# Performance work log

Hardware: AMD Instinct MI355X
Metric: run time of the kernel (lower is better)

## Reference

```python
import jax, jax.numpy as jnp
import numpy as np

B, T, F, V, NTXT = 32, 1, 1, 729, 64
DIM, DIM_LLM = 1152, 4096
HEADS, DIM_HEAD, DEPTH, NUM_LATENTS, FF_MULT = 16, 96, 6, 64, 4
INNER = HEADS * DIM_HEAD
FF_INNER = DIM * FF_MULT
SCALE = DIM_HEAD ** -0.5


def _ln(x, w, b, eps=1e-5):
    mu = x.mean(-1, keepdims=True)
    var = ((x - mu) ** 2).mean(-1, keepdims=True)
    return (x - mu) * jax.lax.rsqrt(var + eps) * w + b


def setup_inputs() -> dict:
    key = jax.random.key(0)
    ks = jax.random.split(key, 12)
    w = lambda k, shape: jax.random.normal(k, shape, dtype=jnp.float32) * 0.02
    return {
        "x": jax.random.normal(ks[0], (B, T, F, V, DIM), dtype=jnp.float32),
        "text_embeds": jax.random.normal(ks[1], (B, NTXT, DIM_LLM), dtype=jnp.float32),
        "latents": jax.random.normal(ks[2], (NUM_LATENTS, DIM), dtype=jnp.float32),
        "txt_w1": w(ks[3], (DIM_LLM, DIM)),
        "txt_b1": jnp.zeros((DIM,), jnp.float32),
        "txt_w2": w(ks[4], (DIM, DIM)),
        "txt_b2": jnp.zeros((DIM,), jnp.float32),
        "nm_w": jnp.ones((DEPTH, DIM), jnp.float32),
        "nm_b": jnp.zeros((DEPTH, DIM), jnp.float32),
        "nl_w": jnp.ones((DEPTH, DIM), jnp.float32),
        "nl_b": jnp.zeros((DEPTH, DIM), jnp.float32),
        "Wq": w(ks[5], (DEPTH, DIM, INNER)),
        "Wkv": w(ks[6], (DEPTH, DIM, 2 * INNER)),
        "Wo": w(ks[7], (DEPTH, INNER, DIM)),
        "ffln_w": jnp.ones((DEPTH, DIM), jnp.float32),
        "ffln_b": jnp.zeros((DEPTH, DIM), jnp.float32),
        "ff_w1": w(ks[8], (DEPTH, DIM, FF_INNER)),
        "ff_w2": w(ks[9], (DEPTH, FF_INNER, DIM)),
        "out_ln_w": jnp.ones((DIM,), jnp.float32),
        "out_ln_b": jnp.zeros((DIM,), jnp.float32),
    }


def reference(x, text_embeds, latents, txt_w1, txt_b1, txt_w2, txt_b2,
              nm_w, nm_b, nl_w, nl_b, Wq, Wkv, Wo,
              ffln_w, ffln_b, ff_w1, ff_w2, out_ln_w, out_ln_b):
    b, t, f, v, d = x.shape
    xf = x.reshape(b, t, f * v, d)  # (b, T, F*v, D)
    # text_projection: Linear -> GELU -> Linear
    txt = jax.nn.gelu(text_embeds @ txt_w1 + txt_b1, approximate=False) @ txt_w2 + txt_b2
    lat = jnp.broadcast_to(latents, (b, t, NUM_LATENTS, d))
    lat = jnp.concatenate(
        [lat, jnp.broadcast_to(txt[:, None], (b, t, txt.shape[1], d))], axis=2)
    n2 = lat.shape[2]
    for i in range(DEPTH):
        # PerceiverAttention
        xm = _ln(xf, nm_w[i], nm_b[i])
        lm = _ln(lat, nl_w[i], nl_b[i])
        q = (lm @ Wq[i]).reshape(b, t, n2, HEADS, DIM_HEAD)
        kv = jnp.concatenate([xm, lm], axis=2) @ Wkv[i]
        k, v_ = jnp.split(kv, 2, axis=-1)
        nk = k.shape[2]
        k = k.reshape(b, t, nk, HEADS, DIM_HEAD)
        v_ = v_.reshape(b, t, nk, HEADS, DIM_HEAD)
        sim = jnp.einsum('btihd,btjhd->bthij', q * SCALE, k)
        attn = jax.nn.softmax(sim, axis=-1)  # stable softmax == amax subtract + softmax
        out = jnp.einsum('bthij,btjhd->btihd', attn, v_).reshape(b, t, n2, INNER) @ Wo[i]
        lat = out + lat
        # FeedForward: LN -> Linear -> GELU -> Linear, residual
        lat = jax.nn.gelu(_ln(lat, ffln_w[i], ffln_b[i]) @ ff_w1[i],
                          approximate=False) @ ff_w2[i] + lat
    lat = lat[:, :, :NUM_LATENTS, :]
    return _ln(lat, out_ln_w, out_ln_b)
```

## Files before the change

### kernel.cpp

```cpp
#include <hip/hip_runtime.h>
#include <hip/hip_bf16.h>
#include <math.h>


typedef __attribute__((ext_vector_type(4))) float f32x4;
typedef __attribute__((ext_vector_type(8))) short bf16x8;
typedef unsigned int u32;

#define DEV __device__ __forceinline__

DEV float bf2f(short s){ union{u32 u; float f;} v; v.u = ((u32)(unsigned short)s) << 16; return v.f; }
DEV short f2bf(float f){
  union{float f; u32 u;} v; v.f = f;
  u32 r = (v.u + 0x7FFFu + ((v.u >> 16) & 1u)) >> 16;
  return (short)r;
}

DEV u32 lds_off(const short* p){
  return (u32)(uintptr_t)(__attribute__((address_space(3))) const short*)p;
}
template<int OFF>
DEV bf16x8 dsro(u32 addr){
  bf16x8 r;
  asm volatile("ds_read_b128 %0, %1 offset:%2" : "=v"(r) : "v"(addr), "i"(OFF));
  return r;
}

template<int GELU, int BIAS, int OUTF32, int CMAP, int KSPLIT>
__global__ __launch_bounds__(512, 4)
void gemm_v2(const short* __restrict__ A, const short* __restrict__ Bm,
             void* __restrict__ Cv, short* __restrict__ C2,
             const float* __restrict__ bias,
             int K, int lda, int ldb, int ldc,
             int Mvalid, int NBmax, int Nwrite)
{
  __shared__ __align__(16) short LDS[36864];

  int Mb = gridDim.x;
  int nwg = gridDim.x * gridDim.y;
  int bid = blockIdx.y * gridDim.x + blockIdx.x;
  int m0, n0;
  if ((Mb & 7) == 0){
    int mslab = Mb >> 3;
    int c = bid & 7, s = bid >> 3;
    int ml = s % mslab, nl = s / mslab;
    m0 = (c*mslab + ml) * 128;
    n0 = nl * 256;
  } else if ((nwg & 7) == 0){
    int chunk = nwg >> 3;
    int b2 = (bid & 7)*chunk + (bid >> 3);
    int by = b2 / Mb;
    m0 = (b2 - by*Mb) * 128;
    n0 = by * 256;
  } else {
    m0 = blockIdx.x * 128;
    n0 = blockIdx.y * 256;
  }
  int kzoff = KSPLIT ? (int)blockIdx.z * K : 0;

  int tid = threadIdx.x, lane = tid & 63, w = tid >> 6;
  int wr = w >> 2, wc = w & 3;
  int rsel = lane & 15, g4 = lane >> 4;

  int sl = lane >> 3;
  int l  = (lane & 7) ^ sl;
  int lc = (l & 3) * 8;
  int lh = l >> 2;
  const short* gA;
  { int r = m0 + w*8 + sl + lh*64; if (r > Mvalid-1) r = Mvalid-1;
    gA = A + (long)r*lda + lc + kzoff; }
  const short* gB0;
  { int r = n0 + w*8 + sl + lh*128; if (r > NBmax-1) r = NBmax-1;
    gB0 = Bm + (long)r*ldb + lc + kzoff; }
  const short* gB1;
  { int r = n0 + 64 + w*8 + sl + lh*128; if (r > NBmax-1) r = NBmax-1;
    gB1 = Bm + (long)r*ldb + lc + kzoff; }
  char* dA  = (char*)LDS + w*1024;
  char* dB0 = (char*)LDS + 8192  + w*1024;
  char* dB1 = (char*)LDS + 16384 + w*1024;

#define GLDS(src, dst) __builtin_amdgcn_global_load_lds( \
      (const __attribute__((address_space(1))) u32*)(src), \
      (__attribute__((address_space(3))) u32*)(dst), 16, 0, 0)
#define STAGE(bo, tau) do { \
    int kb = (tau)*32; \
    GLDS(gA  + kb, dA  + (bo)); \
    GLDS(gB0 + kb, dB0 + (bo)); \
    GLDS(gB1 + kb, dB1 + (bo)); \
  } while(0)

  u32 base = lds_off(LDS);
  u32 aAddr = base + (u32)(rsel*128 + (((wr*4 + g4) ^ (rsel & 7))*16));
  u32 bAddr = base + 8192u
            + (u32)(((wc & 1)*64 + rsel)*128 + ((((wc >> 1)*4 + g4) ^ (rsel & 7))*16));

  int nt = K >> 5;

  f32x4 acc[4][4];
#pragma unroll
  for (int i=0;i<4;i++)
#pragma unroll
    for (int j=0;j<4;j++) acc[i][j] = (f32x4){0.f,0.f,0.f,0.f};

  STAGE(0u, 0);
  if (nt > 1) STAGE(24576u, 1);

  u32 boCur = 0;
#pragma unroll 1
  for (int t=0; t<nt; ++t){
    if (t == nt-1) { asm volatile("s_waitcnt vmcnt(0)" ::: "memory"); }
    else           { asm volatile("s_waitcnt vmcnt(3)" ::: "memory"); }
    asm volatile("s_barrier" ::: "memory");
    u32 aa = aAddr + boCur, bb = bAddr + boCur;
    bf16x8 af[4], bfr[4];
    af[0]  = dsro<0>(aa);    af[1]  = dsro<2048>(aa);
    af[2]  = dsro<4096>(aa); af[3]  = dsro<6144>(aa);
    bfr[0] = dsro<0>(bb);    bfr[1] = dsro<2048>(bb);
    bfr[2] = dsro<4096>(bb); bfr[3] = dsro<6144>(bb);
    if (t+2 < nt){
      u32 boN2 = boCur + 49152u; if (boN2 >= 73728u) boN2 -= 73728u;
      STAGE(boN2, t+2);
    }
    asm volatile("s_waitcnt lgkmcnt(0)" ::: "memory");
    __builtin_amdgcn_sched_barrier(0);
    __builtin_amdgcn_s_setprio(1);
#pragma unroll
    for (int mi=0; mi<4; mi++)
#pragma unroll
      for (int nn=0; nn<4; nn++)
        acc[mi][nn] = __builtin_amdgcn_mfma_f32_16x16x32_bf16(af[mi], bfr[nn], acc[mi][nn], 0, 0, 0);
    __builtin_amdgcn_s_setprio(0);
    boCur += 24576u; if (boCur == 73728u) boCur = 0;
  }
#undef STAGE
#undef GLDS

  int cq = g4 * 4;
  int csel = rsel;
#pragma unroll
  for (int mi=0; mi<4; mi++){
#pragma unroll
    for (int nn=0; nn<4; nn++){
#pragma unroll
      for (int j=0; j<4; j++){
        int gm = m0 + wr*64 + mi*16 + cq + j;
        int gn = n0 + wc*64 + nn*16 + csel;
        if (gm < Mvalid && gn < Nwrite){
          float v = acc[mi][nn][j];
          if (BIAS) v += bias[gn];
          if (GELU) v = 0.5f*v*(1.0f + erff(v*0.70710678118654752f));
          if (CMAP == 0){
            long off = (long)gm*ldc + gn;
            if (KSPLIT) off += (long)blockIdx.z * ((long)Mvalid * ldc);
            if (OUTF32) ((float*)Cv)[off] = v;
            else        ((short*)Cv)[off] = f2bf(v);
          } else if (CMAP == 1){
            int bb2 = gm / 729;
            int jj = gm - bb2*729;
            ((short*)Cv)[((long)bb2*857 + jj)*3072 + gn] = f2bf(v);
          } else {
            if (gn < 1536){
              ((short*)Cv)[(long)gm*1536 + gn] = f2bf(v * 0.1020620726159657f);
            } else {
              int bb2 = gm >> 7, jj = gm & 127;
              C2[((long)bb2*857 + 729 + jj)*3072 + (gn - 1536)] = f2bf(v);
            }
          }
        }
      }
    }
  }
}

__global__ __launch_bounds__(256)
void red2_ln(float* __restrict__ lat, const float* __restrict__ p, long n,
             short* __restrict__ lm, const float* __restrict__ w,
             const float* __restrict__ b)
{
  const int D = 1152;
  int r = blockIdx.x;
  long rb = (long)r*D;
  int tid = threadIdx.x;
  float s1=0.f, s2=0.f;
  float xv[5];
#pragma unroll
  for (int t=0;t<5;t++){
    int i = tid + t*256;
    float v = 0.f;
    if (i < D){
      v = lat[rb+i] + p[rb+i] + p[n+rb+i];
      lat[rb+i] = v;
    }
    xv[t] = v; s1 += v; s2 += v*v;
  }
  if (!w) return;
#pragma unroll
  for (int o=32;o;o>>=1){ s1 += __shfl_xor(s1,o); s2 += __shfl_xor(s2,o); }
  __shared__ float red[8];
  int wid = tid>>6, lane = tid&63;
  if (lane==0){ red[wid]=s1; red[4+wid]=s2; }
  __syncthreads();
  s1 = red[0]+red[1]+red[2]+red[3];
  s2 = red[4]+red[5]+red[6]+red[7];
  float mu = s1 / D;
  float var = s2 / D - mu*mu;
  float rs = rsqrtf(var + 1e-5f);
#pragma unroll
  for (int t=0;t<5;t++){
    int i = tid + t*256;
    if (i >= D) break;
    lm[rb+i] = f2bf((xv[t]-mu)*rs*w[i] + b[i]);
  }
}

__global__ __launch_bounds__(256)
void flash_attn(const short* __restrict__ qb, const short* __restrict__ kv,
                short* __restrict__ attn)
{
  __shared__ short Kt[96][104];
  __shared__ short Vs[96][104];
  __shared__ short Pb[4][32][104];
  __shared__ float FAC[128];

  int z = blockIdx.x;
  int b = z >> 4, h = z & 15;
  int tid = threadIdx.x;
  int lane = tid & 63;
  int w = tid >> 6;
  int l15 = lane & 15, g4 = lane >> 4;

  bf16x8 qf[2][3];
#pragma unroll
  for (int n=0;n<2;n++)
#pragma unroll
    for (int kf=0;kf<3;kf++)
      qf[n][kf] = *(const bf16x8*)&qb[((long)(b*128 + w*32 + n*16 + l15))*1536
                                     + h*96 + kf*32 + g4*8];

  f32x4 acc[2][6];
#pragma unroll
  for (int i=0;i<2;i++)
#pragma unroll
    for (int j=0;j<6;j++) acc[i][j] = (f32x4){0.f,0.f,0.f,0.f};
  float m_run[2] = {-1e30f, -1e30f};
  float l_run[2] = {0.f, 0.f};

  const short* kvb = kv + (long)b*857*3072 + h*96;
  const short* vvb = kvb + 1536;

  for (int t=0; t<9; ++t){
    int k0 = t*96;
    for (int c = tid; c < 1152; c += 256){
      int r = c / 12;
      int c12 = c - r*12;
      int key = k0 + r; if (key > 856) key = 856;
      *(bf16x8*)&Kt[r][c12*8] = *(const bf16x8*)&kvb[(long)key*3072 + c12*8];
      bf16x8 vv = *(const bf16x8*)&vvb[(long)key*3072 + c12*8];
#pragma unroll
      for (int j=0;j<8;j++) Vs[c12*8 + j][r] = ((short*)&vv)[j];
    }
    __syncthreads();

    f32x4 st[6][2];
#pragma unroll
    for (int m=0;m<6;m++){ st[m][0]=(f32x4){0,0,0,0}; st[m][1]=(f32x4){0,0,0,0}; }
#pragma unroll
    for (int kf=0;kf<3;kf++){
      bf16x8 af[6];
#pragma unroll
      for (int m=0;m<6;m++) af[m] = *(const bf16x8*)&Kt[m*16 + l15][kf*32 + g4*8];
#pragma unroll
      for (int m=0;m<6;m++){
        st[m][0] = __builtin_amdgcn_mfma_f32_16x16x32_bf16(af[m], qf[0][kf], st[m][0], 0,0,0);
        st[m][1] = __builtin_amdgcn_mfma_f32_16x16x32_bf16(af[m], qf[1][kf], st[m][1], 0,0,0);
      }
    }

    if (k0 + 96 > 857){
#pragma unroll
      for (int m=0;m<6;m++)
#pragma unroll
        for (int j=0;j<4;j++){
          if (k0 + m*16 + g4*4 + j > 856){ st[m][0][j] = -1e30f; st[m][1][j] = -1e30f; }
        }
    }

#pragma unroll
    for (int n=0;n<2;n++){
      float mx = -1e30f;
#pragma unroll
      for (int m=0;m<6;m++)
#pragma unroll
        for (int j=0;j<4;j++) mx = fmaxf(mx, st[m][n][j]);
      mx = fmaxf(mx, __shfl_xor(mx, 16));
      mx = fmaxf(mx, __shfl_xor(mx, 32));
      float mn = fmaxf(m_run[n], mx);
      float f  = __expf(m_run[n] - mn);
      m_run[n] = mn;
      float s = 0.f;
#pragma unroll
      for (int m=0;m<6;m++)
#pragma unroll
        for (int j=0;j<4;j++){
          float e = __expf(st[m][n][j] - mn);
          st[m][n][j] = e; s += e;
        }
      s += __shfl_xor(s, 16);
      s += __shfl_xor(s, 32);
      l_run[n] = l_run[n]*f + s;
      if (g4 == 0) FAC[w*32 + n*16 + l15] = f;
    }

#pragma unroll
    for (int m=0;m<6;m++)
#pragma unroll
      for (int n=0;n<2;n++){
        short4 pk;
        pk.x = f2bf(st[m][n][0]); pk.y = f2bf(st[m][n][1]);
        pk.z = f2bf(st[m][n][2]); pk.w = f2bf(st[m][n][3]);
        *(short4*)&Pb[w][n*16 + l15][m*16 + g4*4] = pk;
      }

    {
      float4 fj0 = *(const float4*)&FAC[w*32 +  0 + g4*4];
      float4 fj1 = *(const float4*)&FAC[w*32 + 16 + g4*4];
#pragma unroll
      for (int nn=0;nn<6;nn++){
        acc[0][nn][0] *= fj0.x; acc[0][nn][1] *= fj0.y;
        acc[0][nn][2] *= fj0.z; acc[0][nn][3] *= fj0.w;
        acc[1][nn][0] *= fj1.x; acc[1][nn][1] *= fj1.y;
        acc[1][nn][2] *= fj1.z; acc[1][nn][3] *= fj1.w;
      }
    }

#pragma unroll
    for (int kf=0;kf<3;kf++){
      bf16x8 pa0 = *(const bf16x8*)&Pb[w][ 0 + l15][kf*32 + g4*8];
      bf16x8 pa1 = *(const bf16x8*)&Pb[w][16 + l15][kf*32 + g4*8];
#pragma unroll
      for (int nn=0;nn<6;nn++){
        bf16x8 vb = *(const bf16x8*)&Vs[nn*16 + l15][kf*32 + g4*8];
        acc[0][nn] = __builtin_amdgcn_mfma_f32_16x16x32_bf16(pa0, vb, acc[0][nn], 0,0,0);
        acc[1][nn] = __builtin_amdgcn_mfma_f32_16x16x32_bf16(pa1, vb, acc[1][nn], 0,0,0);
      }
    }
    __syncthreads();
  }

  if (g4 == 0){
    FAC[w*32 +  0 + l15] = 1.0f / l_run[0];
    FAC[w*32 + 16 + l15] = 1.0f / l_run[1];
  }
  float4 li0 = *(const float4*)&FAC[w*32 +  0 + g4*4];
  float4 li1 = *(const float4*)&FAC[w*32 + 16 + g4*4];
  float li[2][4] = {{li0.x,li0.y,li0.z,li0.w},{li1.x,li1.y,li1.z,li1.w}};
#pragma unroll
  for (int mo=0;mo<2;mo++)
#pragma unroll
    for (int nn=0;nn<6;nn++)
#pragma unroll
      for (int j=0;j<4;j++){
        int q = w*32 + mo*16 + g4*4 + j;
        int d = nn*16 + l15;
        attn[((long)(b*128+q))*1536 + h*96 + d] = f2bf(acc[mo][nn][j]*li[mo][j]);
      }
}

template<int GELU, int BIAS, int RES, int OUTF32>
__global__ __launch_bounds__(256)
void gemm_t(const short* __restrict__ A, const short* __restrict__ B,
            void* __restrict__ C, const float* __restrict__ bias,
            const float* __restrict__ res,
            int K, int lda, int ldb, int ldc,
            int Mvalid, int NBmax, int Nwrite,
            int zdiv, long sA1, long sA2, long sB1, long sB2, long sC1, long sC2,
            float scale)
{
  __shared__ __align__(16) short As[2][128*32];
  __shared__ __align__(16) short Bs[2][128*32];

  int z = blockIdx.z;
  int zq = z / zdiv, zr = z - zq*zdiv;
  const short* Ab = A + zq*sA1 + zr*sA2;
  const short* Bb = B + zq*sB1 + zr*sB2;
  long cOff = zq*sC1 + zr*sC2;
  int m0 = blockIdx.y * 128;
  int n0 = blockIdx.x * 128;
  int tid = threadIdx.x;
  int lane = tid & 63;
  int w = tid >> 6;
  int wm = (w >> 1) * 64, wn = (w & 1) * 64;

  int sr = lane >> 2;
  int sc = (lane & 3) * 8;
  int ar0 = m0 + w*32 + sr;
  int br0 = n0 + w*32 + sr;

  int raA0 = ar0;      if (raA0 > Mvalid-1) raA0 = Mvalid-1;
  int raA1 = ar0 + 16; if (raA1 > Mvalid-1) raA1 = Mvalid-1;
  int rbB0 = br0;      if (rbB0 > NBmax-1) rbB0 = NBmax-1;
  int rbB1 = br0 + 16; if (rbB1 > NBmax-1) rbB1 = NBmax-1;
  const short* gA0 = Ab + (long)raA0*lda + sc;
  const short* gA1 = Ab + (long)raA1*lda + sc;
  const short* gB0 = Bb + (long)rbB0*ldb + sc;
  const short* gB1 = Bb + (long)rbB1*ldb + sc;
  int ldsRow0 = (w*32)*32;
  int ldsRow1 = (w*32 + 16)*32;

  f32x4 acc[4][4];
#pragma unroll
  for (int i=0;i<4;i++)
#pragma unroll
    for (int j=0;j<4;j++) acc[i][j] = (f32x4){0.f,0.f,0.f,0.f};

  auto stage = [&](int buf, int kb){
    __builtin_amdgcn_global_load_lds(
        (const __attribute__((address_space(1))) u32*)(gA0 + kb),
        (__attribute__((address_space(3))) u32*)(&As[buf][ldsRow0]), 16, 0, 0);
    __builtin_amdgcn_global_load_lds(
        (const __attribute__((address_space(1))) u32*)(gA1 + kb),
        (__attribute__((address_space(3))) u32*)(&As[buf][ldsRow1]), 16, 0, 0);
    __builtin_amdgcn_global_load_lds(
        (const __attribute__((address_space(1))) u32*)(gB0 + kb),
        (__attribute__((address_space(3))) u32*)(&Bs[buf][ldsRow0]), 16, 0, 0);
    __builtin_amdgcn_global_load_lds(
        (const __attribute__((address_space(1))) u32*)(gB1 + kb),
        (__attribute__((address_space(3))) u32*)(&Bs[buf][ldsRow1]), 16, 0, 0);
  };

  int nt = K >> 5;
  stage(0, 0);
  __syncthreads();

  int kq = (lane >> 4) * 8;
  int rsel = lane & 15;
  int cur = 0;
  for (int t = 0; t < nt; ++t){
    if (t + 1 < nt) stage(cur ^ 1, (t+1)*32);

    bf16x8 af[4], bfr[4];
#pragma unroll
    for (int m=0;m<4;m++) af[m]  = *(const bf16x8*)&As[cur][(wm + m*16 + rsel)*32 + kq];
#pragma unroll
    for (int n=0;n<4;n++) bfr[n] = *(const bf16x8*)&Bs[cur][(wn + n*16 + rsel)*32 + kq];
#pragma unroll
    for (int m=0;m<4;m++)
#pragma unroll
      for (int n=0;n<4;n++)
        acc[m][n] = __builtin_amdgcn_mfma_f32_16x16x32_bf16(af[m], bfr[n], acc[m][n], 0, 0, 0);

    __syncthreads();
    cur ^= 1;
  }

  int cq = (lane >> 4) * 4;
  int csel = lane & 15;
#pragma unroll
  for (int m=0;m<4;m++){
#pragma unroll
    for (int n=0;n<4;n++){
#pragma unroll
      for (int j=0;j<4;j++){
        int gm = m0 + wm + m*16 + cq + j;
        int gn = n0 + wn + n*16 + csel;
        if (gm < Mvalid && gn < Nwrite){
          float v = acc[m][n][j] * scale;
          if (BIAS) v += bias[gn];
          if (GELU) v = 0.5f*v*(1.0f + erff(v*0.70710678118654752f));
          long off = cOff + (long)gm*ldc + gn;
          if (OUTF32){
            float rv = RES ? res[off] : 0.0f;
            ((float*)C)[off] = v + rv;
          } else {
            ((short*)C)[off] = f2bf(v);
          }
        }
      }
    }
  }
}

__global__ __launch_bounds__(256)
void convT(const float* __restrict__ in, short* __restrict__ out,
           int K, int N, const float* __restrict__ s)
{
  __shared__ float tile[32][33];
  int kb = blockIdx.y*32, nb = blockIdx.x*32;
  int tx = threadIdx.x & 31, ty = threadIdx.x >> 5;
  for (int i = ty; i < 32; i += 8){
    int k = kb + i, n = nb + tx;
    float v = 0.f;
    if (k < K && n < N){ v = in[(long)k*N + n]; if (s) v *= s[k]; }
    tile[i][tx] = v;
  }
  __syncthreads();
  for (int i = ty; i < 32; i += 8){
    int n = nb + i, k = kb + tx;
    if (n < N && k < K) out[(long)n*K + k] = f2bf(tile[tx][i]);
  }
}

__global__ __launch_bounds__(256)
void convT_qkv(const float* __restrict__ Wq, const float* __restrict__ Wkv,
               const float* __restrict__ s,
               short* __restrict__ outQ, short* __restrict__ outKx,
               short* __restrict__ outK)
{
  __shared__ float tile[32][33];
  __shared__ float sv[32];
  int b = blockIdx.x;
  int tx = threadIdx.x & 31, ty = threadIdx.x >> 5;
  if (b < 1728){
    int bx = b % 48, byy = b / 48;
    int kb = byy*32, nb = bx*32;
    for (int i = ty; i < 32; i += 8)
      tile[i][tx] = Wq[(long)(kb + i)*1536 + nb + tx];
    __syncthreads();
    for (int i = ty; i < 32; i += 8)
      outQ[(long)(nb + i)*1152 + kb + tx] = f2bf(tile[tx][i]);
  } else {
    int b2 = b - 1728;
    int bx = b2 % 96, byy = b2 / 96;
    int kb = byy*32, nb = bx*32;
    if (threadIdx.x < 32) sv[threadIdx.x] = s[kb + threadIdx.x];
    for (int i = ty; i < 32; i += 8)
      tile[i][tx] = Wkv[(long)(kb + i)*3072 + nb + tx];
    __syncthreads();
    for (int i = ty; i < 32; i += 8){
      float v = tile[tx][i];
      long o = (long)(nb + i)*1152 + kb + tx;
      outK[o]  = f2bf(v);
      outKx[o] = f2bf(v * sv[tx]);
    }
  }
}

__global__ __launch_bounds__(256)
void convT_ffo(const float* __restrict__ Wo, const float* __restrict__ fw1,
               const float* __restrict__ fw2,
               short* __restrict__ outWo, short* __restrict__ outF1,
               short* __restrict__ outF2)
{
  __shared__ float tile[32][33];
  int b = blockIdx.x;
  int tx = threadIdx.x & 31, ty = threadIdx.x >> 5;
  const float* in; short* out; int K, N, kb, nb;
  if (b < 1728){
    in = Wo; out = outWo; K = 1536; N = 1152;
    nb = (b % 36)*32; kb = (b / 36)*32;
  } else if (b < 6912){
    int b2 = b - 1728;
    in = fw1; out = outF1; K = 1152; N = 4608;
    nb = (b2 % 144)*32; kb = (b2 / 144)*32;
  } else {
    int b3 = b - 6912;
    in = fw2; out = outF2; K = 4608; N = 1152;
    nb = (b3 % 36)*32; kb = (b3 / 36)*32;
  }
  for (int i = ty; i < 32; i += 8)
    tile[i][tx] = in[(long)(kb + i)*N + nb + tx];
  __syncthreads();
  for (int i = ty; i < 32; i += 8)
    out[(long)(nb + i)*K + kb + tx] = f2bf(tile[tx][i]);
}

__global__ __launch_bounds__(256)
void biasfold6(const float* __restrict__ Wkv, const float* __restrict__ nm_b,
               float* __restrict__ outb)
{
  int L = blockIdx.y;
  int n = blockIdx.x*256 + threadIdx.x;
  const float* W = Wkv + (size_t)L*1152*3072;
  const float* bvec = nm_b + L*1152;
  float s = 0.f;
  for (int k=0;k<1152;k++) s += bvec[k]*W[(long)k*3072 + n];
  outb[L*3072 + n] = s;
}

__global__ __launch_bounds__(256)
void cvt_bf16x4(const float* __restrict__ in, short* __restrict__ o, long n)
{
  long i = ((long)blockIdx.x*256 + threadIdx.x)*4;
  if (i >= n) return;
  float4 v = *(const float4*)(in + i);
  short4 s4;
  s4.x = f2bf(v.x); s4.y = f2bf(v.y); s4.z = f2bf(v.z); s4.w = f2bf(v.w);
  *(short4*)&o[i] = s4;
}

__global__ __launch_bounds__(256)
void latcopy(const float* __restrict__ latents, float* __restrict__ lat)
{
  int idx = blockIdx.x*256 + threadIdx.x;
  int d = idx % 1152; int j = (idx / 1152) % 64; int b = idx / (1152*64);
  lat[((long)b*128 + j)*1152 + d] = latents[j*1152 + d];
}

template<int OUTF32>
__global__ __launch_bounds__(256)
void ln_k(const float* __restrict__ in, void* __restrict__ outp,
          const float* __restrict__ w, const float* __restrict__ b,
          int grpSel, int grpStride)
{
  const int D = 1152;
  int r = blockIdx.x;
  long ir = (long)(r / grpSel)*grpStride + (r % grpSel);
  const float* x = in + ir*D;
  int tid = threadIdx.x;
  float s1=0.f, s2=0.f;
  float xv[5];
#pragma unroll
  for (int t=0;t<5;t++){
    int i = tid + t*256;
    xv[t] = (i < D) ? x[i] : 0.f;
    s1 += xv[t]; s2 += xv[t]*xv[t];
  }
#pragma unroll
  for (int o=32;o;o>>=1){ s1 += __shfl_xor(s1,o); s2 += __shfl_xor(s2,o); }
  __shared__ float red[8];
  int wid = tid>>6, lane = tid&63;
  if (lane==0){ red[wid]=s1; red[4+wid]=s2; }
  __syncthreads();
  s1 = red[0]+red[1]+red[2]+red[3];
  s2 = red[4]+red[5]+red[6]+red[7];
  float mu = s1 / D;
  float var = s2 / D - mu*mu;
  float rs = rsqrtf(var + 1e-5f);
#pragma unroll
  for (int t=0;t<5;t++){
    int i = tid + t*256;
    if (i >= D) break;
    float v = (xv[t]-mu)*rs;
    if (w) v = v*w[i] + b[i];
    if (OUTF32) ((float*)outp)[(long)r*D + i] = v;
    else        ((short*)outp)[(long)r*D + i] = f2bf(v);
  }
}


extern "C" void kernel_launch(void* const* d_in, const int* in_sizes, int n_in,
                              void* d_out, int out_size, void* d_ws, size_t ws_size,
                              hipStream_t stream)
{
  const float* x      = (const float*)d_in[0];
  const float* tein   = (const float*)d_in[1];
  const float* lat0   = (const float*)d_in[2];
  const float* txt_w1 = (const float*)d_in[3];
  const float* txt_b1 = (const float*)d_in[4];
  const float* txt_w2 = (const float*)d_in[5];
  const float* txt_b2 = (const float*)d_in[6];
  const float* nm_w   = (const float*)d_in[7];
  const float* nm_b   = (const float*)d_in[8];
  const float* nl_w   = (const float*)d_in[9];
  const float* nl_b   = (const float*)d_in[10];
  const float* Wq     = (const float*)d_in[11];
  const float* Wkv    = (const float*)d_in[12];
  const float* Wo     = (const float*)d_in[13];
  const float* ffln_w = (const float*)d_in[14];
  const float* ffln_b = (const float*)d_in[15];
  const float* ff_w1  = (const float*)d_in[16];
  const float* ff_w2  = (const float*)d_in[17];
  const float* oln_w  = (const float*)d_in[18];
  const float* oln_b  = (const float*)d_in[19];
  float* out = (float*)d_out;
  (void)in_sizes; (void)n_in; (void)out_size; (void)ws_size;

  char* base = (char*)d_ws;
  size_t off = 0;
  auto alloc = [&](size_t bytes)->char*{
    char* r = base + off;
    off += (bytes + 255) & ~(size_t)255;
    return r;
  };
  short* wT    = (short*)alloc(4608ULL*1152*2);
  short* wTx   = (short*)alloc(3072ULL*1152*2);
  short* wTo   = (short*)alloc(1152ULL*1536*2);
  short* wTf1  = (short*)alloc(4608ULL*1152*2);
  short* wTf2  = (short*)alloc(1152ULL*4608*2);
  float* biasf = (float*)alloc(6*3072*4);
  float* ppart = (float*)alloc(2ULL*4096*1152*4);
  short* xnorm = (short*)alloc(23328ULL*1152*2);
  float* lat   = (float*)alloc(4096ULL*1152*4);
  short* lm    = (short*)alloc(4096ULL*1152*2);
  short* qb    = (short*)alloc(4096ULL*1536*2);
  short* kv    = (short*)alloc(27424ULL*3072*2);
  short* SP    = (short*)alloc(2048ULL*4096*2 + 2048ULL*1152*2);
  short* attn  = (short*)alloc(4096ULL*1536*2);
  short* ffh   = (short*)alloc(4096ULL*4608*2);
  short* txtin = SP;
  short* txth  = SP + 2048ULL*4096;

  cvt_bf16x4<<<8192,256,0,stream>>>(tein, txtin, 2048LL*4096);
  convT<<<dim3(36,128),256,0,stream>>>(txt_w1, wT, 4096, 1152, nullptr);
  gemm_t<1,1,0,0><<<dim3(9,16,1),256,0,stream>>>(txtin, wT, txth, txt_b1, nullptr,
      4096,4096,4096,1152, 2048,1152,1152, 1, 0,0,0,0,0,0, 1.f);
  convT<<<dim3(36,36),256,0,stream>>>(txt_w2, wT, 1152, 1152, nullptr);
  gemm_t<0,1,0,1><<<dim3(9,1,32),256,0,stream>>>(txth, wT, lat + 64*1152, txt_b2, nullptr,
      1152,1152,1152,1152, 64,1152,1152, 1, 64L*1152,0, 0,0, 128L*1152,0, 1.f);
  latcopy<<<9216,256,0,stream>>>(lat0, lat);

  ln_k<0><<<23328,256,0,stream>>>(x, xnorm, nullptr, nullptr, 1<<28, 0);
  ln_k<0><<<4096,256,0,stream>>>(lat, lm, nl_w, nl_b, 1<<28, 0);
  biasfold6<<<dim3(12,6),256,0,stream>>>(Wkv, nm_b, biasf);

  for (int L=0; L<6; L++){
    const float* WqL  = Wq    + (size_t)L*1152*1536;
    const float* WkvL = Wkv   + (size_t)L*1152*3072;
    const float* WoL  = Wo    + (size_t)L*1536*1152;
    const float* fw1  = ff_w1 + (size_t)L*1152*4608;
    const float* fw2  = ff_w2 + (size_t)L*4608*1152;
    int Ln = (L+1 < 6) ? (L+1) : 5;

    convT_qkv<<<5184,256,0,stream>>>(WqL, WkvL, nm_w + L*1152,
        wT, wTx, wT + 1536*1152);

    gemm_v2<0,0,0,2,0><<<dim3(32,18),512,0,stream>>>(lm, wT, qb, kv, nullptr,
        1152,1152,1152,0, 4096, 4608, 4608);

    gemm_v2<0,1,0,1,0><<<dim3(184,12),512,0,stream>>>(xnorm, wTx, kv, nullptr,
        biasf + L*3072, 1152,1152,1152,0, 23328, 3072, 3072);

    flash_attn<<<512,256,0,stream>>>(qb, kv, attn);

    convT_ffo<<<12096,256,0,stream>>>(WoL, fw1, fw2, wTo, wTf1, wTf2);

    gemm_v2<0,0,1,0,1><<<dim3(32,5,2),512,0,stream>>>(attn, wTo, ppart, nullptr, nullptr,
        768,1536,1536,1152, 4096, 1152, 1152);
    red2_ln<<<4096,256,0,stream>>>(lat, ppart, 4096L*1152, lm,
        ffln_w + L*1152, ffln_b + L*1152);

    gemm_v2<1,0,0,0,0><<<dim3(32,18),512,0,stream>>>(lm, wTf1, ffh, nullptr, nullptr,
        1152,1152,1152,4608, 4096, 4608, 4608);
    gemm_v2<0,0,1,0,1><<<dim3(32,5,2),512,0,stream>>>(ffh, wTf2, ppart, nullptr, nullptr,
        2304,4608,4608,1152, 4096, 1152, 1152);
    red2_ln<<<4096,256,0,stream>>>(lat, ppart, 4096L*1152, lm,
        (L+1 < 6) ? (nl_w + Ln*1152) : nullptr, nl_b + Ln*1152);
  }

  ln_k<1><<<2048,256,0,stream>>>(lat, out, oln_w, oln_b, 64, 128);
}
```

Measured before the change: 3.670 ms.

## Merge per-layer weight transposes and fuse Q/KV GEMMs into one launch

Combines the two per-layer weight conversion kernels into a single launch covering Wq, Wkv, Wo and both FF weights. Replaces the two separate GEMM launches, one for the latent Q/KV projection and one for the x KV projection, with a single grouped GEMM kernel. That kernel assigns blocks to either problem by block index, remaps block order into XCD-strided slabs, and uses a triple-buffered global-to-LDS pipeline. The aim is to cut launch overhead and tail underutilisation and to improve L2 locality, at the cost of a more specialised kernel with hard-coded shapes.

```diff
diff --git a/kernel.cpp b/kernel.cpp
--- a/kernel.cpp
+++ b/kernel.cpp
@@ -172,6 +172,143 @@
   }
 }
 
+__global__ __launch_bounds__(512, 4)
+void gemm_qkvx(const short* __restrict__ lm, const short* __restrict__ xnorm,
+               const short* __restrict__ wTq, const short* __restrict__ wTx,
+               short* __restrict__ qb, short* __restrict__ kv,
+               const float* __restrict__ biasL)
+{
+  __shared__ __align__(16) short LDS[36864];
+
+  int bid = blockIdx.x;
+  int which = (bid >= 576);
+  const short* A; const short* Bm;
+  int m0, n0, Mvalid, NBmax;
+  if (!which){
+    int mslab = 4;
+    int c = bid & 7, s = bid >> 3;
+    m0 = (c*mslab + s % mslab) * 128;
+    n0 = (s / mslab) * 256;
+    A = lm; Bm = wTq; Mvalid = 4096; NBmax = 4608;
+  } else {
+    int local = bid - 576;
+    int mslab = 23;
+    int c = local & 7, s = local >> 3;
+    m0 = (c*mslab + s % mslab) * 128;
+    n0 = (s / mslab) * 256;
+    A = xnorm; Bm = wTx; Mvalid = 23328; NBmax = 3072;
+  }
+
+  int tid = threadIdx.x, lane = tid & 63, w = tid >> 6;
+  int wr = w >> 2, wc = w & 3;
+  int rsel = lane & 15, g4 = lane >> 4;
+
+  int sl = lane >> 3;
+  int l  = (lane & 7) ^ sl;
+  int lc = (l & 3) * 8;
+  int lh = l >> 2;
+  const short* gA;
+  { int r = m0 + w*8 + sl + lh*64; if (r > Mvalid-1) r = Mvalid-1;
+    gA = A + (long)r*1152 + lc; }
+  const short* gB0;
+  { int r = n0 + w*8 + sl + lh*128; if (r > NBmax-1) r = NBmax-1;
+    gB0 = Bm + (long)r*1152 + lc; }
+  const short* gB1;
+  { int r = n0 + 64 + w*8 + sl + lh*128; if (r > NBmax-1) r = NBmax-1;
+    gB1 = Bm + (long)r*1152 + lc; }
+  char* dA  = (char*)LDS + w*1024;
+  char* dB0 = (char*)LDS + 8192  + w*1024;
+  char* dB1 = (char*)LDS + 16384 + w*1024;
+
+#define GLDS(src, dst) __builtin_amdgcn_global_load_lds( \
+      (const __attribute__((address_space(1))) u32*)(src), \
+      (__attribute__((address_space(3))) u32*)(dst), 16, 0, 0)
+#define STAGE(bo, tau) do { \
+    int kb = (tau)*32; \
+    GLDS(gA  + kb, dA  + (bo)); \
+    GLDS(gB0 + kb, dB0 + (bo)); \
+    GLDS(gB1 + kb, dB1 + (bo)); \
+  } while(0)
+
+  u32 base = lds_off(LDS);
+  u32 aAddr = base + (u32)(rsel*128 + (((wr*4 + g4) ^ (rsel & 7))*16));
+  u32 bAddr = base + 8192u
+            + (u32)(((wc & 1)*64 + rsel)*128 + ((((wc >> 1)*4 + g4) ^ (rsel & 7))*16));
+
+  const int nt = 36;
+
+  f32x4 acc[4][4];
+#pragma unroll
+  for (int i=0;i<4;i++)
+#pragma unroll
+    for (int j=0;j<4;j++) acc[i][j] = (f32x4){0.f,0.f,0.f,0.f};
+
+  STAGE(0u, 0);
+  STAGE(24576u, 1);
+
+  u32 boCur = 0;
+#pragma unroll 1
+  for (int t=0; t<nt; ++t){
+    if (t == nt-1) { asm volatile("s_waitcnt vmcnt(0)" ::: "memory"); }
+    else           { asm volatile("s_waitcnt vmcnt(3)" ::: "memory"); }
+    asm volatile("s_barrier" ::: "memory");
+    u32 aa = aAddr + boCur, bb = bAddr + boCur;
+    bf16x8 af[4], bfr[4];
+    af[0]  = dsro<0>(aa);    af[1]  = dsro<2048>(aa);
+    af[2]  = dsro<4096>(aa); af[3]  = dsro<6144>(aa);
+    bfr[0] = dsro<0>(bb);    bfr[1] = dsro<2048>(bb);
+    bfr[2] = dsro<4096>(bb); bfr[3] = dsro<6144>(bb);
+    if (t+2 < nt){
+      u32 boN2 = boCur + 49152u; if (boN2 >= 73728u) boN2 -= 73728u;
+      STAGE(boN2, t+2);
+    }
+    asm volatile("s_waitcnt lgkmcnt(0)" ::: "memory");
+    __builtin_amdgcn_sched_barrier(0);
+    __builtin_amdgcn_s_setprio(1);
+#pragma unroll
+    for (int mi=0; mi<4; mi++)
+#pragma unroll
+      for (int nn=0; nn<4; nn++)
+        acc[mi][nn] = __builtin_amdgcn_mfma_f32_16x16x32_bf16(af[mi], bfr[nn], acc[mi][nn], 0, 0, 0);
+    __builtin_amdgcn_s_setprio(0);
+    boCur += 24576u; if (boCur == 73728u) boCur = 0;
+  }
+#undef STAGE
+#undef GLDS
+
+  int cq = g4 * 4;
+  int csel = rsel;
+#pragma unroll
+  for (int mi=0; mi<4; mi++){
+#pragma unroll
+    for (int nn=0; nn<4; nn++){
+#pragma unroll
+      for (int j=0; j<4; j++){
+        int gm = m0 + wr*64 + mi*16 + cq + j;
+        int gn = n0 + wc*64 + nn*16 + csel;
+        if (!which){
+          if (gm < 4096 && gn < 4608){
+            float v = acc[mi][nn][j];
+            if (gn < 1536){
+              qb[(long)gm*1536 + gn] = f2bf(v * 0.1020620726159657f);
+            } else {
+              int bb2 = gm >> 7, jj = gm & 127;
+              kv[((long)bb2*857 + 729 + jj)*3072 + (gn - 1536)] = f2bf(v);
+            }
+          }
+        } else {
+          if (gm < 23328 && gn < 3072){
+            float v = acc[mi][nn][j] + biasL[gn];
+            int bb2 = gm / 729;
+            int jj = gm - bb2*729;
+            kv[((long)bb2*857 + jj)*3072 + gn] = f2bf(v);
+          }
+        }
+      }
+    }
+  }
+}
+
 __global__ __launch_bounds__(256)
 void red2_ln(float* __restrict__ lat, const float* __restrict__ p, long n,
              short* __restrict__ lm, const float* __restrict__ w,
@@ -501,10 +638,13 @@
 }
 
 __global__ __launch_bounds__(256)
-void convT_qkv(const float* __restrict__ Wq, const float* __restrict__ Wkv,
-               const float* __restrict__ s,
-               short* __restrict__ outQ, short* __restrict__ outKx,
-               short* __restrict__ outK)
+void convT_wall(const float* __restrict__ Wq, const float* __restrict__ Wkv,
+                const float* __restrict__ s,
+                const float* __restrict__ Wo, const float* __restrict__ fw1,
+                const float* __restrict__ fw2,
+                short* __restrict__ outQ, short* __restrict__ outKx,
+                short* __restrict__ outK, short* __restrict__ outWo,
+                short* __restrict__ outF1, short* __restrict__ outF2)
 {
   __shared__ float tile[32][33];
   __shared__ float sv[32];
@@ -518,7 +658,7 @@
     __syncthreads();
     for (int i = ty; i < 32; i += 8)
       outQ[(long)(nb + i)*1152 + kb + tx] = f2bf(tile[tx][i]);
-  } else {
+  } else if (b < 5184){
     int b2 = b - 1728;
     int bx = b2 % 96, byy = b2 / 96;
     int kb = byy*32, nb = bx*32;
@@ -532,36 +672,27 @@
       outK[o]  = f2bf(v);
       outKx[o] = f2bf(v * sv[tx]);
     }
-  }
-}
-
-__global__ __launch_bounds__(256)
-void convT_ffo(const float* __restrict__ Wo, const float* __restrict__ fw1,
-               const float* __restrict__ fw2,
-               short* __restrict__ outWo, short* __restrict__ outF1,
-               short* __restrict__ outF2)
-{
-  __shared__ float tile[32][33];
-  int b = blockIdx.x;
-  int tx = threadIdx.x & 31, ty = threadIdx.x >> 5;
-  const float* in; short* out; int K, N, kb, nb;
-  if (b < 1728){
-    in = Wo; out = outWo; K = 1536; N = 1152;
-    nb = (b % 36)*32; kb = (b / 36)*32;
-  } else if (b < 6912){
-    int b2 = b - 1728;
-    in = fw1; out = outF1; K = 1152; N = 4608;
-    nb = (b2 % 144)*32; kb = (b2 / 144)*32;
   } else {
-    int b3 = b - 6912;
-    in = fw2; out = outF2; K = 4608; N = 1152;
-    nb = (b3 % 36)*32; kb = (b3 / 36)*32;
-  }
-  for (int i = ty; i < 32; i += 8)
-    tile[i][tx] = in[(long)(kb + i)*N + nb + tx];
-  __syncthreads();
-  for (int i = ty; i < 32; i += 8)
-    out[(long)(nb + i)*K + kb + tx] = f2bf(tile[tx][i]);
+    const float* in; short* out; int K, N, kb, nb;
+    if (b < 6912){
+      int b3 = b - 5184;
+      in = Wo; out = outWo; K = 1536; N = 1152;
+      nb = (b3 % 36)*32; kb = (b3 / 36)*32;
+    } else if (b < 12096){
+      int b4 = b - 6912;
+      in = fw1; out = outF1; K = 1152; N = 4608;
+      nb = (b4 % 144)*32; kb = (b4 / 144)*32;
+    } else {
+      int b5 = b - 12096;
+      in = fw2; out = outF2; K = 4608; N = 1152;
+      nb = (b5 % 36)*32; kb = (b5 / 36)*32;
+    }
+    for (int i = ty; i < 32; i += 8)
+      tile[i][tx] = in[(long)(kb + i)*N + nb + tx];
+    __syncthreads();
+    for (int i = ty; i < 32; i += 8)
+      out[(long)(nb + i)*K + kb + tx] = f2bf(tile[tx][i]);
+  }
 }
 
 __global__ __launch_bounds__(256)
@@ -711,18 +842,12 @@
     const float* fw2  = ff_w2 + (size_t)L*4608*1152;
     int Ln = (L+1 < 6) ? (L+1) : 5;
 
-    convT_qkv<<<5184,256,0,stream>>>(WqL, WkvL, nm_w + L*1152,
-        wT, wTx, wT + 1536*1152);
-
-    gemm_v2<0,0,0,2,0><<<dim3(32,18),512,0,stream>>>(lm, wT, qb, kv, nullptr,
-        1152,1152,1152,0, 4096, 4608, 4608);
-
-    gemm_v2<0,1,0,1,0><<<dim3(184,12),512,0,stream>>>(xnorm, wTx, kv, nullptr,
-        biasf + L*3072, 1152,1152,1152,0, 23328, 3072, 3072);
+    convT_wall<<<17280,256,0,stream>>>(WqL, WkvL, nm_w + L*1152, WoL, fw1, fw2,
+        wT, wTx, wT + 1536*1152, wTo, wTf1, wTf2);
+
+    gemm_qkvx<<<2784,512,0,stream>>>(lm, xnorm, wT, wTx, qb, kv, biasf + L*3072);
 
     flash_attn<<<512,256,0,stream>>>(qb, kv, attn);
-
-    convT_ffo<<<12096,256,0,stream>>>(WoL, fw1, fw2, wTo, wTf1, wTf2);
 
     gemm_v2<0,0,1,0,1><<<dim3(32,5,2),512,0,stream>>>(attn, wTo, ppart, nullptr, nullptr,
         768,1536,1536,1152, 4096, 1152, 1152);
```

New measurement: 3.760 ms. 1.02x slower.
